# Optimization experiments

Hardware: AMD Instinct MI355X
Metric: run time of the kernel (lower is better)

## Reference

```python
import jax, jax.numpy as jnp
import numpy as np

N_NODES, N_EDGES, N_GRAPHS = 100000, 1600000, 1000
DIN, DMID, DGLOB, DOUT = 128, 128, 64, 2


def setup_inputs() -> dict:
    key = jax.random.key(0)
    ks = jax.random.split(key, 12)
    x = jax.random.normal(ks[0], (N_NODES, DIN), dtype=jnp.float32)
    edge_index = jax.random.randint(ks[1], (2, N_EDGES), 0, N_NODES, dtype=jnp.int64 if jax.config.jax_enable_x64 else jnp.int32)
    u = jax.random.normal(ks[2], (N_GRAPHS, DGLOB), dtype=jnp.float32)
    batch = jnp.sort(jax.random.randint(ks[3], (N_NODES,), 0, N_GRAPHS))
    s = 1.0 / np.sqrt(DMID)
    W1 = jax.random.normal(ks[4], (DIN, DMID), dtype=jnp.float32) * s
    b1 = jnp.zeros((DMID,), dtype=jnp.float32)
    W2 = jax.random.normal(ks[5], (DMID, DMID), dtype=jnp.float32) * s
    b2 = jnp.zeros((DMID,), dtype=jnp.float32)
    Wh1 = jax.random.normal(ks[6], (DMID + DGLOB, DMID), dtype=jnp.float32) * s
    bh1 = jnp.zeros((DMID,), dtype=jnp.float32)
    Wh2 = jax.random.normal(ks[7], (DMID, DOUT), dtype=jnp.float32) * s
    bh2 = jnp.zeros((DOUT,), dtype=jnp.float32)
    return {"x": x, "edge_index": edge_index, "u": u, "batch": batch,
            "batch_size": N_GRAPHS, "W1": W1, "b1": b1, "W2": W2, "b2": b2,
            "Wh1": Wh1, "bh1": bh1, "Wh2": Wh2, "bh2": bh2}


def _gcn_conv(x, W, b, row, col, norm, n):
    # PyG GCNConv: linear transform then symmetric-normalized scatter-add
    h = x @ W                                    # [N, dmid]
    msg = norm[:, None] * h[row]                 # gather along source nodes
    out = jax.ops.segment_sum(msg, col, num_segments=n)  # scatter to dst
    return out + b


def reference(x, edge_index, u, batch, batch_size, W1, b1, W2, b2, Wh1, bh1, Wh2, bh2):
    n = x.shape[0]
    # add self-loops (GCNConv default, edge_weight=None -> all-ones weights)
    loop = jnp.arange(n, dtype=edge_index.dtype)
    row = jnp.concatenate([edge_index[0], loop])
    col = jnp.concatenate([edge_index[1], loop])
    deg = jax.ops.segment_sum(jnp.ones_like(col, dtype=x.dtype), col, num_segments=n)
    dinv = jnp.where(deg > 0, jax.lax.rsqrt(jnp.maximum(deg, 1e-12)), 0.0)
    norm = dinv[row] * dinv[col]                 # D^-1/2 A D^-1/2, shared by both layers

    h = jax.nn.relu(_gcn_conv(x, W1, b1, row, col, norm, n))
    h = jax.nn.relu(_gcn_conv(h, W2, b2, row, col, norm, n))

    # mean pool per graph
    sums = jax.ops.segment_sum(h, batch, num_segments=batch_size)
    cnt = jax.ops.segment_sum(jnp.ones((n,), dtype=h.dtype), batch, num_segments=batch_size)
    graph_emb = sums / jnp.maximum(cnt, 1.0)[:, None]

    hcat = jnp.concatenate([graph_emb, u], axis=-1)
    # head MLP (dropout in eval mode = identity)
    out = jax.nn.relu(hcat @ Wh1 + bh1) @ Wh2 + bh2
    return out
```

## Files before the change

kernel.cpp:

```cpp
#include <hip/hip_runtime.h>
#include <hip/hip_bf16.h>

#define NN 100000
#define NE 1600000
#define NG 1000
#define NBK 196
#define BSH 9
#define SLOT 10240
#define SLOTC 12288

typedef short short8 __attribute__((ext_vector_type(8)));
typedef float f32x4 __attribute__((ext_vector_type(4)));
typedef float f32x2 __attribute__((ext_vector_type(2)));

static inline int cdiv(int a, int b) { return (a + b - 1) / b; }

__device__ __forceinline__ unsigned short f2b(float f) {
    unsigned int u = __float_as_uint(f);
    u += 0x7fff + ((u >> 16) & 1);
    return (unsigned short)(u >> 16);
}
__device__ __forceinline__ unsigned int pack2(float lo, float hi) {
    return (unsigned int)f2b(lo) | ((unsigned int)f2b(hi) << 16);
}

template <int W>
__device__ __forceinline__ f32x2 f8_2f(unsigned int v) {
    return __builtin_amdgcn_cvt_pk_f32_fp8((int)v, W);
}
__device__ __forceinline__ unsigned int f2f8_lo(float a, float b, unsigned int old) {
    return (unsigned int)__builtin_amdgcn_cvt_pk_fp8_f32(a, b, (int)old, false);
}
__device__ __forceinline__ unsigned int f2f8_hi(float a, float b, unsigned int old) {
    return (unsigned int)__builtin_amdgcn_cvt_pk_fp8_f32(a, b, (int)old, true);
}
__device__ __forceinline__ unsigned char f2f8s(float a) {
    return (unsigned char)(__builtin_amdgcn_cvt_pk_fp8_f32(a, a, 0, false) & 0xFF);
}

__global__ __launch_bounds__(256) void k_prep(const float* __restrict__ W1,
                                              const float* __restrict__ W2,
                                              const float* __restrict__ b1,
                                              const float* __restrict__ b2,
                                              unsigned short* __restrict__ Wt1,
                                              unsigned char* __restrict__ Wt2p,
                                              float* __restrict__ b1p,
                                              float* __restrict__ b2p,
                                              int* __restrict__ gcur,
                                              const int* __restrict__ batch,
                                              int* __restrict__ gstart,
                                              unsigned char* __restrict__ Hs8,
                                              unsigned char* __restrict__ Hg2) {
    int b = blockIdx.x, t = threadIdx.x;
    if (b < 128) {
        if (t < 128) {
            Wt1[b * 128 + t] = f2b(W1[t * 128 + b]);
        } else {
            int q = t - 128;
            int c = (q & 7) * 16 + (q >> 3);
            Wt2p[b * 128 + q] = f2f8s(W2[c * 128 + b]);
        }
    } else if (b == 128) {
        if (t < NBK) gcur[t] = t * SLOT;
        if (t < 128) {
            int c = (t & 7) * 16 + (t >> 3);
            b1p[t] = b1[c];
            b2p[t] = b2[c];
        }
        if (t >= 128 && t < 136) {
            uint4 z; z.x = 0u; z.y = 0u; z.z = 0u; z.w = 0u;
            ((uint4*)(Hs8 + (size_t)NN * 128))[t - 128] = z;
        }
        if (t >= 136 && t < 144) {
            uint4 z; z.x = 0u; z.y = 0u; z.z = 0u; z.w = 0u;
            ((uint4*)(Hg2 + (size_t)NN * 128))[t - 136] = z;
        }
    } else {
        int n = (b - 129) * 256 + t;
        if (n <= NN) {
            int cur = (n == NN) ? NG : batch[n];
            int prev = (n == 0) ? -1 : batch[n - 1];
            for (int g = prev + 1; g <= cur; g++) gstart[g] = n;
        }
    }
}

__global__ __launch_bounds__(256) void k_bin2(const int* __restrict__ row,
                                              const int* __restrict__ col,
                                              int* __restrict__ gcur,
                                              unsigned int* __restrict__ tmp) {
    __shared__ unsigned int ent[4000];
    __shared__ unsigned int srt[4000];
    __shared__ unsigned char bkt[4000];
    __shared__ unsigned char bky[4000];
    __shared__ int cnt[NBK];
    __shared__ int gbase[NBK];
    __shared__ int lbase[NBK];
    __shared__ int sh[256];
    int t = threadIdx.x;
    if (t < NBK) cnt[t] = 0;
    __syncthreads();
    const int q0 = blockIdx.x * 1000;
    const int4* col4 = (const int4*)col;
    const int4* row4 = (const int4*)row;
#pragma unroll
    for (int it = 0; it < 4; it++) {
        int idx = it * 256 + t;
        if (idx < 1000) {
            int4 c = col4[q0 + idx];
            int4 r = row4[q0 + idx];
            int d, b;
            d = c.x; b = d >> BSH; atomicAdd(&cnt[b], 1);
            ent[idx * 4 + 0] = ((unsigned int)(d & 511) << 17) | (unsigned int)r.x;
            bkt[idx * 4 + 0] = (unsigned char)b;
            d = c.y; b = d >> BSH; atomicAdd(&cnt[b], 1);
            ent[idx * 4 + 1] = ((unsigned int)(d & 511) << 17) | (unsigned int)r.y;
            bkt[idx * 4 + 1] = (unsigned char)b;
            d = c.z; b = d >> BSH; atomicAdd(&cnt[b], 1);
            ent[idx * 4 + 2] = ((unsigned int)(d & 511) << 17) | (unsigned int)r.z;
            bkt[idx * 4 + 2] = (unsigned char)b;
            d = c.w; b = d >> BSH; atomicAdd(&cnt[b], 1);
            ent[idx * 4 + 3] = ((unsigned int)(d & 511) << 17) | (unsigned int)r.w;
            bkt[idx * 4 + 3] = (unsigned char)b;
        }
    }
    __syncthreads();
    int v = (t < NBK) ? cnt[t] : 0;
    sh[t] = v;
    __syncthreads();
    for (int d = 1; d < 256; d <<= 1) {
        int u = (t >= d) ? sh[t - d] : 0;
        __syncthreads();
        sh[t] += u;
        __syncthreads();
    }
    if (t < NBK) {
        lbase[t] = sh[t] - v;
        gbase[t] = atomicAdd(&gcur[t], v);
        cnt[t] = sh[t] - v;
    }
    __syncthreads();
#pragma unroll
    for (int it = 0; it < 16; it++) {
        int i = it * 256 + t;
        if (i < 4000) {
            int b = bkt[i];
            int p = atomicAdd(&cnt[b], 1);
            srt[p] = ent[i];
            bky[p] = (unsigned char)b;
        }
    }
    __syncthreads();
#pragma unroll
    for (int it = 0; it < 16; it++) {
        int i = it * 256 + t;
        if (i < 4000) {
            int b = bky[i];
            tmp[gbase[b] + (i - lbase[b])] = srt[i];
        }
    }
}

__global__ __launch_bounds__(1024) void k_bucket(const unsigned int* __restrict__ tmp,
                                                 const int* __restrict__ gcur,
                                                 unsigned int* __restrict__ meta,
                                                 float* __restrict__ dinv,
                                                 int* __restrict__ csr_src) {
    __shared__ unsigned int sent[SLOT];
    __shared__ int cnt[512];
    __shared__ int loff[512];
    __shared__ int send[512];
    __shared__ int sh[256];
    int b = blockIdx.x, t = threadIdx.x;
    int j0 = b << BSH;
    int nd = min(512, NN - j0);
    int rb = b * SLOT;
    int rbc = b * SLOTC;
    int m = gcur[b] - rb;
    if (t < 512) cnt[t] = 0;
    __syncthreads();
    for (int i = t; i < m; i += 1024) {
        unsigned int e = tmp[rb + i];
        sent[i] = e;
        atomicAdd(&cnt[e >> 17], 1);
    }
    __syncthreads();
    int r0 = 0, r1 = 0, p0 = 0, ts = 0;
    if (t < 256) {
        r0 = cnt[2 * t]; r1 = cnt[2 * t + 1];
        p0 = (r0 + 7) & ~7;
        int p1 = (r1 + 7) & ~7;
        ts = p0 + p1;
        sh[t] = ts;
    }
    __syncthreads();
    for (int d = 1; d < 256; d <<= 1) {
        int u = (t >= d && t < 256) ? sh[t - d] : 0;
        __syncthreads();
        if (t < 256) sh[t] += u;
        __syncthreads();
    }
    if (t < 256) {
        int ex = sh[t] - ts;
        loff[2 * t] = ex;
        loff[2 * t + 1] = ex + p0;
    }
    __syncthreads();
    for (int j = t; j < nd; j += 1024) {
        int o = rbc + loff[j];
        int dg = cnt[j];
        int dgp = (dg + 7) & ~7;
        meta[j0 + j] = (unsigned int)o | ((unsigned int)dgp << 22);
        send[j] = o + dgp;
        dinv[j0 + j] = rsqrtf((float)(dg + 1));
        cnt[j] = o;
    }
    __syncthreads();
    for (int i = t; i < m; i += 1024) {
        unsigned int e = sent[i];
        int d = e >> 17;
        int s = (int)(e & 0x1FFFFu);
        int p = atomicAdd(&cnt[d], 1);
        csr_src[p] = s;
    }
    __syncthreads();
    for (int j = t; j < nd; j += 1024) {
        int pe = send[j];
        for (int p = cnt[j]; p < pe; p++) csr_src[p] = NN;
    }
}

__global__ __launch_bounds__(256) void k_gemm1(const float* __restrict__ X,
                                               const unsigned short* __restrict__ Wt,
                                               const float* __restrict__ dinv,
                                               unsigned char* __restrict__ Hs8) {
    __shared__ __align__(16) unsigned short Ws[128 * 128];
    int t = threadIdx.x;
#pragma unroll
    for (int i = 0; i < 8; i++) {
        int id = t + i * 256;
        int n = id >> 4, c = id & 15;
        *(short8*)((char*)Ws + n * 256 + ((c ^ (n & 15)) << 4)) =
            *(const short8*)(Wt + n * 128 + c * 8);
    }
    __syncthreads();

    int lane = t & 63, wid = t >> 6;
    int n16 = lane & 15, quad = lane >> 4;
    int row_base = blockIdx.x * 128 + wid * 32;

    short8 a[2][4];
#pragma unroll
    for (int rt = 0; rt < 2; rt++) {
        int r = row_base + rt * 16 + n16;
        if (r > NN - 1) r = NN - 1;
        const float* ap = X + (size_t)r * 128 + quad * 8;
#pragma unroll
        for (int ks = 0; ks < 4; ks++) {
            float4 v0 = *(const float4*)(ap + ks * 32);
            float4 v1 = *(const float4*)(ap + ks * 32 + 4);
            uint4 up;
            up.x = pack2(v0.x, v0.y); up.y = pack2(v0.z, v0.w);
            up.z = pack2(v1.x, v1.y); up.w = pack2(v1.z, v1.w);
            a[rt][ks] = *(short8*)&up;
        }
    }

    f32x4 acc[2][8];
#pragma unroll
    for (int rt = 0; rt < 2; rt++)
#pragma unroll
        for (int ct = 0; ct < 8; ct++)
            acc[rt][ct] = (f32x4){0.f, 0.f, 0.f, 0.f};

#pragma unroll
    for (int ks = 0; ks < 4; ks++) {
#pragma unroll
        for (int ct = 0; ct < 8; ct++) {
            short8 b = *(const short8*)((const char*)Ws +
                        (ct * 16 + n16) * 256 + ((((ks << 2) + quad) ^ n16) << 4));
            acc[0][ct] = __builtin_amdgcn_mfma_f32_16x16x32_bf16(a[0][ks], b, acc[0][ct], 0, 0, 0);
            acc[1][ct] = __builtin_amdgcn_mfma_f32_16x16x32_bf16(a[1][ks], b, acc[1][ct], 0, 0, 0);
        }
    }

#pragma unroll
    for (int rt = 0; rt < 2; rt++) {
#pragma unroll
        for (int reg = 0; reg < 4; reg++) {
            int row = row_base + rt * 16 + quad * 4 + reg;
            if (row < NN) {
                float di = dinv[row];
                unsigned int u0 = 0, u1 = 0;
                u0 = f2f8_lo(acc[rt][0][reg] * di, acc[rt][1][reg] * di, u0);
                u0 = f2f8_hi(acc[rt][2][reg] * di, acc[rt][3][reg] * di, u0);
                u1 = f2f8_lo(acc[rt][4][reg] * di, acc[rt][5][reg] * di, u1);
                u1 = f2f8_hi(acc[rt][6][reg] * di, acc[rt][7][reg] * di, u1);
                uint2 o; o.x = u0; o.y = u1;
                ((uint2*)(Hs8 + (size_t)row * 128))[n16] = o;
            }
        }
    }
}

template <int FUSE>
__global__ __launch_bounds__(256) void k_agg(const unsigned char* __restrict__ Hb,
                                             const unsigned int* __restrict__ meta,
                                             const int* __restrict__ csr_src,
                                             const float* __restrict__ dinv,
                                             const float* __restrict__ biasp,
                                             const unsigned char* __restrict__ Wt2p,
                                             unsigned char* __restrict__ outp) {
    __shared__ __align__(16) unsigned char sm[FUSE ? (128 * 128 + 16 * 128) : 16];
    int t = threadIdx.x;
    if (FUSE) {
#pragma unroll
        for (int i = 0; i < 8; i++) {
            int id = t + i * 256;
            int n = id >> 4, c = id & 15;
            *(uint2*)(sm + n * 128 + ((c ^ (n & 15)) << 3)) =
                *(const uint2*)(Wt2p + n * 128 + c * 8);
        }
    }
    int sub = t >> 4;
    int node = blockIdx.x * 16 + sub;
    int li = t & 15;
    unsigned lo8 = (unsigned)li * 8u;
    unsigned int md = meta[node];
    int base = (int)(md & 0x3FFFFFu);
    int degp = (int)(md >> 22);
    f32x2 A0 = {0.f, 0.f}, A1 = {0.f, 0.f}, A2 = {0.f, 0.f}, A3 = {0.f, 0.f};
#define LDH(idx) (*(const uint2*)(Hb + (unsigned)(idx) * 128u + lo8))
#define ACC8(V) { \
        A0 += f8_2f<0>((V).x); A1 += f8_2f<1>((V).x); \
        A2 += f8_2f<0>((V).y); A3 += f8_2f<1>((V).y); }
    uint2 v = LDH(node);
    const int4* ip = (const int4*)(csr_src + base);
    int4 i0 = ip[0], i1 = ip[1], i2 = ip[2], i3 = ip[3];
    ACC8(v)
    for (int e0 = 0; e0 < degp; e0 += 16) {
        uint2 w0 = LDH(i0.x), w1 = LDH(i0.y), w2 = LDH(i0.z), w3 = LDH(i0.w);
        uint2 w4 = LDH(i1.x), w5 = LDH(i1.y), w6 = LDH(i1.z), w7 = LDH(i1.w);
        uint2 w8 = {0, 0}, w9 = {0, 0}, wA = {0, 0}, wB = {0, 0};
        uint2 wC = {0, 0}, wD = {0, 0}, wE = {0, 0}, wF = {0, 0};
        if (e0 + 8 < degp) {
            w8 = LDH(i2.x); w9 = LDH(i2.y); wA = LDH(i2.z); wB = LDH(i2.w);
            wC = LDH(i3.x); wD = LDH(i3.y); wE = LDH(i3.z); wF = LDH(i3.w);
        }
        if (e0 + 16 < degp) {
            const int4* np = (const int4*)(csr_src + base + e0 + 16);
            i0 = np[0]; i1 = np[1]; i2 = np[2]; i3 = np[3];
        }
        ACC8(w0) ACC8(w1) ACC8(w2) ACC8(w3)
        ACC8(w4) ACC8(w5) ACC8(w6) ACC8(w7)
        ACC8(w8) ACC8(w9) ACC8(wA) ACC8(wB)
        ACC8(wC) ACC8(wD) ACC8(wE) ACC8(wF)
    }
#undef ACC8
#undef LDH
    float di = dinv[node];
    const float4* b4 = (const float4*)biasp;
    float4 bA = b4[li * 2], bB = b4[li * 2 + 1];
    float r0 = fmaxf(fmaf(di, A0[0], bA.x), 0.f);
    float r1 = fmaxf(fmaf(di, A0[1], bA.y), 0.f);
    float r2 = fmaxf(fmaf(di, A1[0], bA.z), 0.f);
    float r3 = fmaxf(fmaf(di, A1[1], bA.w), 0.f);
    float r4 = fmaxf(fmaf(di, A2[0], bB.x), 0.f);
    float r5 = fmaxf(fmaf(di, A2[1], bB.y), 0.f);
    float r6 = fmaxf(fmaf(di, A3[0], bB.z), 0.f);
    float r7 = fmaxf(fmaf(di, A3[1], bB.w), 0.f);
    unsigned int u0 = 0, u1 = 0;
    u0 = f2f8_lo(r0, r1, u0); u0 = f2f8_hi(r2, r3, u0);
    u1 = f2f8_lo(r4, r5, u1); u1 = f2f8_hi(r6, r7, u1);
    uint2 o; o.x = u0; o.y = u1;
    if (!FUSE) {
        *(uint2*)(outp + (unsigned)node * 128u + lo8) = o;
        return;
    }
    *(uint2*)(sm + 16384 + sub * 128 + (((li ^ sub) & 15) << 3)) = o;
    __syncthreads();
    int wid = t >> 6, lane = t & 63;
    if (wid < 2) {
        int n16 = lane & 15, quad = lane >> 4;
        f32x4 acc[4];
#pragma unroll
        for (int j = 0; j < 4; j++) acc[j] = (f32x4){0.f, 0.f, 0.f, 0.f};
        int ct0 = wid * 4;
#pragma unroll
        for (int ks = 0; ks < 4; ks++) {
            uint2 av = *(const uint2*)(sm + 16384 + n16 * 128 +
                                       ((((ks << 2) + quad) ^ n16) << 3));
            long aa = __builtin_bit_cast(long, av);
#pragma unroll
            for (int j = 0; j < 4; j++) {
                uint2 bv = *(const uint2*)(sm + ((ct0 + j) * 16 + n16) * 128 +
                                           ((((ks << 2) + quad) ^ n16) << 3));
                long bb = __builtin_bit_cast(long, bv);
                acc[j] = __builtin_amdgcn_mfma_f32_16x16x32_fp8_fp8(aa, bb, acc[j], 0, 0, 0);
            }
        }
#pragma unroll
        for (int reg = 0; reg < 4; reg++) {
            int row = blockIdx.x * 16 + quad * 4 + reg;
            float d2 = dinv[row];
            unsigned int g = f2f8_lo(acc[0][reg] * d2, acc[1][reg] * d2, 0);
            g = f2f8_hi(acc[2][reg] * d2, acc[3][reg] * d2, g);
            *(unsigned int*)(outp + (size_t)row * 128 + n16 * 8 + ct0) = g;
        }
    }
}

__global__ __launch_bounds__(256) void k_poolhead(const unsigned char* __restrict__ A,
                                                  const int* __restrict__ gstart,
                                                  const float* __restrict__ u,
                                                  const float* __restrict__ Wh1,
                                                  const float* __restrict__ bh1,
                                                  const float* __restrict__ Wh2,
                                                  const float* __restrict__ bh2,
                                                  float* __restrict__ out) {
    int g = blockIdx.x, t = threadIdx.x;
    int start = gstart[g];
    int end = gstart[g + 1];

    int li = t & 7;
    int ri = t >> 3;
    float acc[16];
#pragma unroll
    for (int j = 0; j < 16; j++) acc[j] = 0.f;
    f32x2 p;
    for (int i = start + ri; i < end; i += 32) {
        uint4 v = ((const uint4*)A)[(size_t)i * 8 + li];
#define UP(VV, base) p = f8_2f<0>(VV); acc[base] += p.x; acc[base+1] += p.y; \
                     p = f8_2f<1>(VV); acc[base+2] += p.x; acc[base+3] += p.y;
        UP(v.x, 0) UP(v.y, 4) UP(v.z, 8) UP(v.w, 12)
#undef UP
    }
#pragma unroll
    for (int j = 0; j < 16; j++) {
        acc[j] += __shfl_xor(acc[j], 8);
        acc[j] += __shfl_xor(acc[j], 16);
        acc[j] += __shfl_xor(acc[j], 32);
    }
    __shared__ float part[4][128];
    __shared__ float hc[192];
    __shared__ float tt[128];
    __shared__ float red[8];
    int w = t >> 6;
    if ((t & 63) < 8) {
#pragma unroll
        for (int j = 0; j < 16; j++) part[w][li * 16 + j] = acc[j];
    }
    __syncthreads();
    float cntf = (float)max(end - start, 1);
    if (t < 128) {
        int q = (t & 15) * 8 + (t >> 4);
        hc[t] = (part[0][q] + part[1][q] + part[2][q] + part[3][q]) / cntf;
    } else if (t < 192) {
        hc[t] = u[g * 64 + (t - 128)];
    }
    __syncthreads();
    if (t < 128) {
        float a2 = bh1[t];
#pragma unroll 8
        for (int k = 0; k < 192; k++) a2 = fmaf(hc[k], Wh1[k * 128 + t], a2);
        tt[t] = fmaxf(a2, 0.f);
    }
    __syncthreads();
    float p0 = 0.f, p1 = 0.f;
    if (t < 128) {
        float vv = tt[t];
        p0 = vv * Wh2[t * 2];
        p1 = vv * Wh2[t * 2 + 1];
    }
#pragma unroll
    for (int d = 32; d >= 1; d >>= 1) {
        p0 += __shfl_xor(p0, d);
        p1 += __shfl_xor(p1, d);
    }
    if ((t & 63) == 0) { red[w * 2] = p0; red[w * 2 + 1] = p1; }
    __syncthreads();
    if (t == 0) out[g * 2 + 0] = bh2[0] + red[0] + red[2];
    if (t == 1) out[g * 2 + 1] = bh2[1] + red[1] + red[3];
}

extern "C" void kernel_launch(void* const* d_in, const int* in_sizes, int n_in,
                              void* d_out, int out_size, void* d_ws, size_t ws_size,
                              hipStream_t stream) {
    const float* x   = (const float*)d_in[0];
    const int*   ei  = (const int*)d_in[1];
    const int*   row = ei;
    const int*   col = ei + NE;
    const float* u   = (const float*)d_in[2];
    const int*   batch = (const int*)d_in[3];
    const float* W1  = (const float*)d_in[5];
    const float* b1  = (const float*)d_in[6];
    const float* W2  = (const float*)d_in[7];
    const float* b2  = (const float*)d_in[8];
    const float* Wh1 = (const float*)d_in[9];
    const float* bh1 = (const float*)d_in[10];
    const float* Wh2 = (const float*)d_in[11];
    const float* bh2 = (const float*)d_in[12];
    float* out = (float*)d_out;

    char* ws = (char*)d_ws;
    size_t o = 0;
    auto alloc = [&](size_t bytes) -> void* {
        void* p = ws + o;
        o += (bytes + 511) & ~(size_t)511;
        return p;
    };
    unsigned char*  Hs8 = (unsigned char*)alloc((size_t)(NN + 1) * 128);
    unsigned char*  Hg2 = (unsigned char*)alloc((size_t)(NN + 1) * 128);
    unsigned char*  A2b = (unsigned char*)alloc((size_t)NN * 128);
    unsigned short* Wt1 = (unsigned short*)alloc((size_t)128 * 128 * 2);
    unsigned char*  Wt2p= (unsigned char*)alloc((size_t)128 * 128);
    float* b1p    = (float*)alloc((size_t)128 * 4);
    float* b2p    = (float*)alloc((size_t)128 * 4);
    float* dinv   = (float*)alloc((size_t)NN * 4);
    unsigned int* meta = (unsigned int*)alloc((size_t)NN * 4);
    int*   csr_src= (int*)alloc((size_t)NBK * SLOTC * 4 + 512);
    unsigned int* tmp = (unsigned int*)alloc((size_t)NBK * SLOT * 4);
    int*   gcur   = (int*)alloc((size_t)256 * 4);
    int*   gstart = (int*)alloc((size_t)(NG + 1) * 4);

    k_prep<<<129 + cdiv(NN + 1, 256), 256, 0, stream>>>(W1, W2, b1, b2, Wt1, Wt2p,
                                                        b1p, b2p, gcur, batch, gstart,
                                                        Hs8, Hg2);
    k_bin2<<<400, 256, 0, stream>>>(row, col, gcur, tmp);
    k_bucket<<<NBK, 1024, 0, stream>>>(tmp, gcur, meta, dinv, csr_src);

    k_gemm1<<<cdiv(NN, 128), 256, 0, stream>>>(x, Wt1, dinv, Hs8);
    k_agg<1><<<NN / 16, 256, 0, stream>>>(Hs8, meta, csr_src, dinv, b1p, Wt2p, Hg2);
    k_agg<0><<<NN / 16, 256, 0, stream>>>(Hg2, meta, csr_src, dinv, b2p, nullptr, A2b);

    k_poolhead<<<NG, 256, 0, stream>>>(A2b, gstart, u, Wh1, bh1, Wh2, bh2, out);
}
```

Measured before the change: 231.6 us.

## Fuse mean-pool segment sum into second aggregation via atomics

The second aggregation kernel no longer writes an FP8 node-feature buffer. Each block reduces its 16 nodes' fp32 outputs in shared memory by graph id, using the sorted batch, and atomically adds the partial sums into a zeroed per-graph sum buffer. The head kernel then reads those sums instead of re-reading all node rows. This removes a 12.8MB write and read plus the pooling pass, but adds float atomics (with nondeterministic summation order) and a zero-fill of the sum buffer in the prep kernel.

Result: no change. 227.8 us (median of 3 runs) (-1.7%).

```diff
diff --git a/kernel.cpp b/kernel.cpp
--- a/kernel.cpp
+++ b/kernel.cpp
@@ -50,7 +50,8 @@
                                               const int* __restrict__ batch,
                                               int* __restrict__ gstart,
                                               unsigned char* __restrict__ Hs8,
-                                              unsigned char* __restrict__ Hg2) {
+                                              unsigned char* __restrict__ Hg2,
+                                              float* __restrict__ gsum) {
     int b = blockIdx.x, t = threadIdx.x;
     if (b < 128) {
         if (t < 128) {
@@ -75,12 +76,18 @@
             uint4 z; z.x = 0u; z.y = 0u; z.z = 0u; z.w = 0u;
             ((uint4*)(Hg2 + (size_t)NN * 128))[t - 136] = z;
         }
-    } else {
+    } else if (b < 520) {
         int n = (b - 129) * 256 + t;
         if (n <= NN) {
             int cur = (n == NN) ? NG : batch[n];
             int prev = (n == 0) ? -1 : batch[n - 1];
             for (int g = prev + 1; g <= cur; g++) gstart[g] = n;
+        }
+    } else {
+        int i = (b - 520) * 256 + t;
+        if (i < NG * 32) {
+            uint4 z; z.x = 0u; z.y = 0u; z.z = 0u; z.w = 0u;
+            ((uint4*)gsum)[i] = z;
         }
     }
 }
@@ -303,17 +310,19 @@
     }
 }
 
-template <int FUSE>
+template <int MODE>
 __global__ __launch_bounds__(256) void k_agg(const unsigned char* __restrict__ Hb,
                                              const unsigned int* __restrict__ meta,
                                              const int* __restrict__ csr_src,
                                              const float* __restrict__ dinv,
                                              const float* __restrict__ biasp,
                                              const unsigned char* __restrict__ Wt2p,
-                                             unsigned char* __restrict__ outp) {
-    __shared__ __align__(16) unsigned char sm[FUSE ? (128 * 128 + 16 * 128) : 16];
+                                             unsigned char* __restrict__ outp,
+                                             const int* __restrict__ batch,
+                                             float* __restrict__ gsum) {
+    __shared__ __align__(16) unsigned char sm[MODE == 1 ? 18432 : 8512];
     int t = threadIdx.x;
-    if (FUSE) {
+    if (MODE == 1) {
 #pragma unroll
         for (int i = 0; i < 8; i++) {
             int id = t + i * 256;
@@ -369,14 +378,34 @@
     float r5 = fmaxf(fmaf(di, A2[1], bB.y), 0.f);
     float r6 = fmaxf(fmaf(di, A3[0], bB.z), 0.f);
     float r7 = fmaxf(fmaf(di, A3[1], bB.w), 0.f);
+    if (MODE == 2) {
+        float* buf = (float*)sm;
+        int* gid = (int*)(sm + 8448);
+        int wb = sub * 132 + li * 8;
+        buf[wb + 0] = r0; buf[wb + 1] = r1; buf[wb + 2] = r2; buf[wb + 3] = r3;
+        buf[wb + 4] = r4; buf[wb + 5] = r5; buf[wb + 6] = r6; buf[wb + 7] = r7;
+        if (li == 0) gid[sub] = batch[node];
+        __syncthreads();
+        if (t < 128) {
+            int cg = gid[0];
+            float s = buf[t];
+#pragma unroll
+            for (int r = 1; r < 16; r++) {
+                int g2 = gid[r];
+                if (g2 != cg) {
+                    atomicAdd(&gsum[cg * 128 + t], s);
+                    cg = g2; s = 0.f;
+                }
+                s += buf[r * 132 + t];
+            }
+            atomicAdd(&gsum[cg * 128 + t], s);
+        }
+        return;
+    }
     unsigned int u0 = 0, u1 = 0;
     u0 = f2f8_lo(r0, r1, u0); u0 = f2f8_hi(r2, r3, u0);
     u1 = f2f8_lo(r4, r5, u1); u1 = f2f8_hi(r6, r7, u1);
     uint2 o; o.x = u0; o.y = u1;
-    if (!FUSE) {
-        *(uint2*)(outp + (unsigned)node * 128u + lo8) = o;
-        return;
-    }
     *(uint2*)(sm + 16384 + sub * 128 + (((li ^ sub) & 15) << 3)) = o;
     __syncthreads();
     int wid = t >> 6, lane = t & 63;
@@ -410,51 +439,22 @@
     }
 }
 
-__global__ __launch_bounds__(256) void k_poolhead(const unsigned char* __restrict__ A,
-                                                  const int* __restrict__ gstart,
-                                                  const float* __restrict__ u,
-                                                  const float* __restrict__ Wh1,
-                                                  const float* __restrict__ bh1,
-                                                  const float* __restrict__ Wh2,
-                                                  const float* __restrict__ bh2,
-                                                  float* __restrict__ out) {
+__global__ __launch_bounds__(256) void k_head(const float* __restrict__ gsum,
+                                              const int* __restrict__ gstart,
+                                              const float* __restrict__ u,
+                                              const float* __restrict__ Wh1,
+                                              const float* __restrict__ bh1,
+                                              const float* __restrict__ Wh2,
+                                              const float* __restrict__ bh2,
+                                              float* __restrict__ out) {
     int g = blockIdx.x, t = threadIdx.x;
-    int start = gstart[g];
-    int end = gstart[g + 1];
-
-    int li = t & 7;
-    int ri = t >> 3;
-    float acc[16];
-#pragma unroll
-    for (int j = 0; j < 16; j++) acc[j] = 0.f;
-    f32x2 p;
-    for (int i = start + ri; i < end; i += 32) {
-        uint4 v = ((const uint4*)A)[(size_t)i * 8 + li];
-#define UP(VV, base) p = f8_2f<0>(VV); acc[base] += p.x; acc[base+1] += p.y; \
-                     p = f8_2f<1>(VV); acc[base+2] += p.x; acc[base+3] += p.y;
-        UP(v.x, 0) UP(v.y, 4) UP(v.z, 8) UP(v.w, 12)
-#undef UP
-    }
-#pragma unroll
-    for (int j = 0; j < 16; j++) {
-        acc[j] += __shfl_xor(acc[j], 8);
-        acc[j] += __shfl_xor(acc[j], 16);
-        acc[j] += __shfl_xor(acc[j], 32);
-    }
-    __shared__ float part[4][128];
     __shared__ float hc[192];
     __shared__ float tt[128];
     __shared__ float red[8];
-    int w = t >> 6;
-    if ((t & 63) < 8) {
-#pragma unroll
-        for (int j = 0; j < 16; j++) part[w][li * 16 + j] = acc[j];
-    }
-    __syncthreads();
-    float cntf = (float)max(end - start, 1);
+    float cntf = (float)max(gstart[g + 1] - gstart[g], 1);
     if (t < 128) {
         int q = (t & 15) * 8 + (t >> 4);
-        hc[t] = (part[0][q] + part[1][q] + part[2][q] + part[3][q]) / cntf;
+        hc[t] = gsum[g * 128 + q] / cntf;
     } else if (t < 192) {
         hc[t] = u[g * 64 + (t - 128)];
     }
@@ -466,6 +466,7 @@
         tt[t] = fmaxf(a2, 0.f);
     }
     __syncthreads();
+    int w = t >> 6;
     float p0 = 0.f, p1 = 0.f;
     if (t < 128) {
         float vv = tt[t];
@@ -511,7 +512,6 @@
     };
     unsigned char*  Hs8 = (unsigned char*)alloc((size_t)(NN + 1) * 128);
     unsigned char*  Hg2 = (unsigned char*)alloc((size_t)(NN + 1) * 128);
-    unsigned char*  A2b = (unsigned char*)alloc((size_t)NN * 128);
     unsigned short* Wt1 = (unsigned short*)alloc((size_t)128 * 128 * 2);
     unsigned char*  Wt2p= (unsigned char*)alloc((size_t)128 * 128);
     float* b1p    = (float*)alloc((size_t)128 * 4);
@@ -522,16 +522,18 @@
     unsigned int* tmp = (unsigned int*)alloc((size_t)NBK * SLOT * 4);
     int*   gcur   = (int*)alloc((size_t)256 * 4);
     int*   gstart = (int*)alloc((size_t)(NG + 1) * 4);
-
-    k_prep<<<129 + cdiv(NN + 1, 256), 256, 0, stream>>>(W1, W2, b1, b2, Wt1, Wt2p,
-                                                        b1p, b2p, gcur, batch, gstart,
-                                                        Hs8, Hg2);
+    float* gsum   = (float*)alloc((size_t)NG * 128 * 4);
+
+    k_prep<<<645, 256, 0, stream>>>(W1, W2, b1, b2, Wt1, Wt2p, b1p, b2p, gcur,
+                                    batch, gstart, Hs8, Hg2, gsum);
     k_bin2<<<400, 256, 0, stream>>>(row, col, gcur, tmp);
     k_bucket<<<NBK, 1024, 0, stream>>>(tmp, gcur, meta, dinv, csr_src);
 
     k_gemm1<<<cdiv(NN, 128), 256, 0, stream>>>(x, Wt1, dinv, Hs8);
-    k_agg<1><<<NN / 16, 256, 0, stream>>>(Hs8, meta, csr_src, dinv, b1p, Wt2p, Hg2);
-    k_agg<0><<<NN / 16, 256, 0, stream>>>(Hg2, meta, csr_src, dinv, b2p, nullptr, A2b);
-
-    k_poolhead<<<NG, 256, 0, stream>>>(A2b, gstart, u, Wh1, bh1, Wh2, bh2, out);
-}
+    k_agg<1><<<NN / 16, 256, 0, stream>>>(Hs8, meta, csr_src, dinv, b1p, Wt2p,
+                                          Hg2, nullptr, nullptr);
+    k_agg<2><<<NN / 16, 256, 0, stream>>>(Hg2, meta, csr_src, dinv, b2p, nullptr,
+                                          nullptr, batch, gsum);
+
+    k_head<<<NG, 256, 0, stream>>>(gsum, gstart, u, Wh1, bh1, Wh2, bh2, out);
+}
```
